# Kernel tuning notes

Measured on AMD Instinct MI355X. Metric: run time of the kernel, lower is better.

The kernel has to match this reference:

```python
import jax, jax.numpy as jnp
import numpy as np

N_NODES = 50000
N_EDGES = 800000
HEADS = 4
NEG_SLOPE = 0.2  # DGL GATConv default and act1 slope


def _gat_layer(x, src, dst, W, al, ar, b, n_nodes, heads, dh):
    # x: [N, Fin] -> proj: [N, H, Dh]
    proj = (x @ W).reshape(n_nodes, heads, dh)
    el = jnp.einsum('nhd,hd->nh', proj, al)  # [N, H]
    er = jnp.einsum('nhd,hd->nh', proj, ar)  # [N, H]
    e = jax.nn.leaky_relu(el[src] + er[dst], NEG_SLOPE)  # [E, H]
    # segment softmax over incoming edges of each dst node
    m = jax.ops.segment_max(e, dst, num_segments=n_nodes)
    m = jnp.where(jnp.isfinite(m), m, jnp.zeros_like(m))
    ex = jnp.exp(e - m[dst])
    s = jax.ops.segment_sum(ex, dst, num_segments=n_nodes)
    alpha = ex / (s[dst] + 1e-9)  # [E, H]
    msg = proj[src] * alpha[:, :, None]  # [E, H, Dh]
    out = jax.ops.segment_sum(msg, dst, num_segments=n_nodes)  # [N, H, Dh]
    return out.reshape(n_nodes, heads * dh) + b


def setup_inputs() -> dict:
    key = jax.random.key(0)
    ks = jax.random.split(key, 10)
    d = {
        'init_emb': jax.random.normal(ks[0], (N_NODES, 300), jnp.float32) * 0.1,
        'W1': jax.random.normal(ks[1], (300, 400), jnp.float32) * (1.0 / np.sqrt(300)),
        'al1': jax.random.normal(ks[2], (HEADS, 100), jnp.float32) * 0.1,
        'ar1': jax.random.normal(ks[3], (HEADS, 100), jnp.float32) * 0.1,
        'b1': jnp.zeros((400,), jnp.float32),
        'W2': jax.random.normal(ks[4], (400, 512), jnp.float32) * (1.0 / np.sqrt(400)),
        'al2': jax.random.normal(ks[5], (HEADS, 128), jnp.float32) * 0.1,
        'ar2': jax.random.normal(ks[6], (HEADS, 128), jnp.float32) * 0.1,
        'b2': jnp.zeros((512,), jnp.float32),
        'src': jax.random.randint(ks[7], (N_EDGES,), 0, N_NODES, jnp.int32),
        'dst': jax.random.randint(ks[8], (N_EDGES,), 0, N_NODES, jnp.int32),
    }
    return d


def reference(init_emb, W1, al1, ar1, b1, W2, al2, ar2, b2, src, dst):
    x = _gat_layer(init_emb, src, dst, W1, al1, ar1, b1, N_NODES, HEADS, 100)  # [N, 400]
    x = jax.nn.leaky_relu(x, NEG_SLOPE)  # act1
    x = _gat_layer(x, src, dst, W2, al2, ar2, b2, N_NODES, HEADS, 128)  # [N, 512]
    return x
```

## Files before the change

kernel.cpp:

```cpp
#include <hip/hip_runtime.h>
#include <math.h>
#include <stdint.h>

#define NN 50000
#define NE 800000
#define HEADS 4
#define MPAD 50048

typedef __attribute__((ext_vector_type(8))) short bf16x8;
typedef __attribute__((ext_vector_type(4))) float f32x4;

__device__ __forceinline__ uint32_t bf16rne(float x) {
  uint32_t b = __float_as_uint(x);
  return (b + 0x7FFFu + ((b >> 16) & 1u)) >> 16;
}
__device__ __forceinline__ float bflo(uint32_t v) {
  return __uint_as_float(v << 16);
}
__device__ __forceinline__ float bfhi(uint32_t v) {
  return __uint_as_float(v & 0xFFFF0000u);
}

__device__ __forceinline__ void pair_write(const float v[8], char* rowp, int q, int x) {
  uint32_t hi[8], lo[8];
#pragma unroll
  for (int j = 0; j < 8; ++j) {
    hi[j] = bf16rne(v[j]);
    float back = __uint_as_float(hi[j] << 16);
    lo[j] = bf16rne(v[j] - back);
  }
  uint4 hp, lp;
  hp.x = hi[0] | (hi[1] << 16);
  hp.y = hi[2] | (hi[3] << 16);
  hp.z = hi[4] | (hi[5] << 16);
  hp.w = hi[6] | (hi[7] << 16);
  lp.x = lo[0] | (lo[1] << 16);
  lp.y = lo[2] | (lo[3] << 16);
  lp.z = lo[4] | (lo[5] << 16);
  lp.w = lo[6] | (lo[7] << 16);
  *(uint4*)(rowp + ((q ^ x) << 4)) = hp;
  *(uint4*)(rowp + (((4 | q) ^ x) << 4)) = lp;
}

__global__ void hist_kernel(const int* __restrict__ dst, int* __restrict__ counts, int n) {
  int i = blockIdx.x * blockDim.x + threadIdx.x;
  if (i < n) atomicAdd(&counts[dst[i]], 1);
}

__global__ void scan_kernel(const int* __restrict__ counts, int* __restrict__ row_ptr,
                            int* __restrict__ cursor, int n) {
  __shared__ int wsum[16];
  const int lane = threadIdx.x & 63;
  const int w = threadIdx.x >> 6;
  int carry = 0;
  for (int start = 0; start < n; start += 1024) {
    int i = start + (int)threadIdx.x;
    int v = (i < n) ? counts[i] : 0;
    int x = v;
#pragma unroll
    for (int off = 1; off < 64; off <<= 1) {
      int t = __shfl_up(x, off);
      if (lane >= off) x += t;
    }
    if (lane == 63) wsum[w] = x;
    __syncthreads();
    if (w == 0 && lane < 16) {
      int s = wsum[lane];
#pragma unroll
      for (int off = 1; off < 16; off <<= 1) {
        int t = __shfl_up(s, off);
        if (lane >= off) s += t;
      }
      wsum[lane] = s;
    }
    __syncthreads();
    int woff = (w > 0) ? wsum[w - 1] : 0;
    int incl = x + woff;
    if (i < n) {
      int val = carry + incl - v;
      row_ptr[i] = val;
      cursor[i] = val;
    }
    carry += wsum[15];
    __syncthreads();
  }
  if (threadIdx.x == 0) row_ptr[n] = carry;
}

__global__ void scatter_kernel(const int* __restrict__ dst, const int* __restrict__ src,
                               int* __restrict__ cursor, int* __restrict__ srcs, int n) {
  int i = blockIdx.x * blockDim.x + threadIdx.x;
  if (i < n) {
    int pos = atomicAdd(&cursor[dst[i]], 1);
    srcs[pos] = src[i];
  }
}

__global__ void prepare_kernel(const float* __restrict__ X, unsigned short* __restrict__ A2,
                               const float* __restrict__ W1, unsigned short* __restrict__ B2a,
                               const float* __restrict__ W2, unsigned short* __restrict__ B2b) {
  const int bid = blockIdx.x;
  const int wv = threadIdx.x >> 6;
  const int t = threadIdx.x & 63;
  const int s = t >> 2, q = t & 3;
  const int kb = s * 32 + q * 8;
  if (bid < 1024) {
    if (t >= 40) return;
    const int nw = 1024 * 4;
    for (int m = bid * 4 + wv; m < MPAD; m += nw) {
      float v[8];
#pragma unroll
      for (int j = 0; j < 8; ++j) {
        int k = kb + j;
        v[j] = (m < NN && k < 300) ? X[(size_t)m * 300 + k] : 0.f;
      }
      pair_write(v, (char*)A2 + (size_t)m * 1280 + s * 128, q, m & 7);
    }
  } else if (bid < 1152) {
    if (t >= 40) return;
    const int n = (bid - 1024) * 4 + wv;
    float v[8];
#pragma unroll
    for (int j = 0; j < 8; ++j) {
      int k = kb + j;
      v[j] = (n < 400 && k < 300) ? W1[(size_t)k * 400 + n] : 0.f;
    }
    pair_write(v, (char*)B2a + (size_t)n * 1280 + s * 128, q, n & 7);
  } else {
    if (t >= 52) return;
    const int n = (bid - 1152) * 4 + wv;
    float v[8];
#pragma unroll
    for (int j = 0; j < 8; ++j) {
      int kp = kb + j;
      int h = kp / 104;
      int d = kp - h * 104;
      v[j] = (d < 100) ? W2[(size_t)(h * 100 + d) * 512 + n] : 0.f;
    }
    pair_write(v, (char*)B2b + (size_t)n * 1664 + s * 128, q, n & 7);
  }
}

__global__ __launch_bounds__(256, 2) void gemm_pairs(
    const unsigned short* __restrict__ A2, const unsigned short* __restrict__ B2,
    unsigned short* __restrict__ Ch, int M, int ksteps, int NstR, int RSc,
    int DHR, int DHP, int magic) {
  __shared__ unsigned short As[8192];
  __shared__ unsigned short Bs[8192];
  const int tid = threadIdx.x;
  const int w = tid >> 6, lane = tid & 63;
  const int wr = w >> 1, wc = w & 1;
  const int ln = lane & 15, quad = lane >> 4;
  const int m0 = blockIdx.y * 128, n0 = blockIdx.x * 128;
  const long strideB = (long)ksteps * 128;

  f32x4 acc[4][4];
#pragma unroll
  for (int mi = 0; mi < 4; ++mi)
#pragma unroll
    for (int ni = 0; ni < 4; ++ni) acc[mi][ni] = (f32x4){0.f, 0.f, 0.f, 0.f};

  const int xa = ln & 7;
  const int gA0 = (quad ^ xa) << 4, gA1 = ((4 | quad) ^ xa) << 4;

  for (int s = 0; s < ksteps; ++s) {
    const long sb = (long)s * 128;
#pragma unroll
    for (int j = 0; j < 4; ++j) {
      const int t16 = w * 4 + j;
      const int row = t16 * 8 + (lane >> 3);
      const int gran = lane & 7;
      const char* gpA = (const char*)A2 + (size_t)(m0 + row) * strideB + sb + gran * 16;
      const char* gpB = (const char*)B2 + (size_t)(n0 + row) * strideB + sb + gran * 16;
      __builtin_amdgcn_global_load_lds(
          (const __attribute__((address_space(1))) void*)gpA,
          (__attribute__((address_space(3))) void*)((char*)As + t16 * 1024), 16, 0, 0);
      __builtin_amdgcn_global_load_lds(
          (const __attribute__((address_space(1))) void*)gpB,
          (__attribute__((address_space(3))) void*)((char*)Bs + t16 * 1024), 16, 0, 0);
    }
    __syncthreads();
    bf16x8 ah[4], alo[4], bh[4], blo[4];
#pragma unroll
    for (int mi = 0; mi < 4; ++mi) {
      const int rA = wr * 64 + mi * 16 + ln;
      ah[mi] = *(const bf16x8*)((const char*)As + rA * 128 + gA0);
      alo[mi] = *(const bf16x8*)((const char*)As + rA * 128 + gA1);
    }
#pragma unroll
    for (int ni = 0; ni < 4; ++ni) {
      const int rB = wc * 64 + ni * 16 + ln;
      bh[ni] = *(const bf16x8*)((const char*)Bs + rB * 128 + gA0);
      blo[ni] = *(const bf16x8*)((const char*)Bs + rB * 128 + gA1);
    }
#pragma unroll
    for (int mi = 0; mi < 4; ++mi)
#pragma unroll
      for (int ni = 0; ni < 4; ++ni)
        acc[mi][ni] = __builtin_amdgcn_mfma_f32_16x16x32_bf16(ah[mi], bh[ni], acc[mi][ni], 0, 0, 0);
#pragma unroll
    for (int mi = 0; mi < 4; ++mi)
#pragma unroll
      for (int ni = 0; ni < 4; ++ni)
        acc[mi][ni] = __builtin_amdgcn_mfma_f32_16x16x32_bf16(ah[mi], blo[ni], acc[mi][ni], 0, 0, 0);
#pragma unroll
    for (int mi = 0; mi < 4; ++mi)
#pragma unroll
      for (int ni = 0; ni < 4; ++ni)
        acc[mi][ni] = __builtin_amdgcn_mfma_f32_16x16x32_bf16(alo[mi], bh[ni], acc[mi][ni], 0, 0, 0);
    __syncthreads();
  }
#pragma unroll
  for (int mi = 0; mi < 4; ++mi) {
#pragma unroll
    for (int r = 0; r < 4; ++r) {
      int gm = m0 + wr * 64 + mi * 16 + quad * 4 + r;
      if (gm < M) {
        unsigned short* crow = Ch + (size_t)gm * RSc;
#pragma unroll
        for (int ni = 0; ni < 4; ++ni) {
          int gn = n0 + wc * 64 + ni * 16 + ln;
          if (gn < NstR) {
            int h = (gn * magic) >> 12;
            int col = h * DHP + (gn - h * DHR);
            crow[col] = (unsigned short)bf16rne(acc[mi][ni][r]);
          }
        }
      }
    }
  }
}

template <int DHR, int DHP>
__global__ void el_er_kernel(const unsigned short* __restrict__ projh,
                             const float* __restrict__ al, const float* __restrict__ ar,
                             float* __restrict__ el, float* __restrict__ er) {
  int t = blockIdx.x * blockDim.x + threadIdx.x;
  if (t >= NN * HEADS) return;
  int h = t & (HEADS - 1);
  int n = t >> 2;
  const unsigned short* pr = projh + (size_t)n * (HEADS * DHP) + (size_t)h * DHP;
  const float* alh = al + h * DHR;
  const float* arh = ar + h * DHR;
  float sl = 0.f, sr = 0.f;
#pragma unroll 4
  for (int d = 0; d < DHR; d += 4) {
    uint2 pv = *(const uint2*)&pr[d];
    float p0 = bflo(pv.x), p1 = bfhi(pv.x), p2 = bflo(pv.y), p3 = bfhi(pv.y);
    float4 av = *(const float4*)&alh[d];
    float4 rv = *(const float4*)&arh[d];
    sl += p0 * av.x + p1 * av.y + p2 * av.z + p3 * av.w;
    sr += p0 * rv.x + p1 * rv.y + p2 * rv.z + p3 * rv.w;
  }
  el[t] = sl;
  er[t] = sr;
}

template <int DHP, int DHR, bool ACT, bool EMIT>
__global__ __launch_bounds__(256) void aggregate4(
    const unsigned short* __restrict__ projh, const float* __restrict__ el,
    const float* __restrict__ er, const float* __restrict__ bias,
    const int* __restrict__ row_ptr, const int* __restrict__ srcs,
    float* __restrict__ out, unsigned short* __restrict__ a2) {
  constexpr int LPH = DHP / 8;
  constexpr int RS = HEADS * DHP * 2;
  const int lane = threadIdx.x & 63;
  const int wid = blockIdx.x * 4 + (threadIdx.x >> 6);
  const int nw = gridDim.x * 4;
  const int e16 = lane >> 2, hp = lane & 3;
  int head;
  if constexpr (LPH == 16) head = lane >> 4;
  else head = (lane * 5) >> 6;
  const int u = lane - head * LPH;
  const bool active = lane < 4 * LPH;
  const int laneByte = active ? head * (DHP * 2) + u * 16 : 0;
  const char* pb = (const char*)projh;

  float bv[8];
  const int d0 = u * 8;
#pragma unroll
  for (int j = 0; j < 8; ++j)
    bv[j] = (active && d0 + j < DHR) ? bias[head * DHR + d0 + j] : 0.f;

  for (int node = wid; node < NN; node += nw) {
    const int beg = row_ptr[node], end = row_ptr[node + 1];
    const float er_p = er[node * 4 + hp];

    float acc[8];
#pragma unroll
    for (int j = 0; j < 8; ++j) acc[j] = 0.f;
    float lsum = 0.f;

    int i = beg;
    int rem = end - beg;
    int sE = 0;
    float elv = 0.f;
    if (rem > 0 && e16 < rem) {
      sE = srcs[i + e16];
      elv = el[sE * 4 + hp];
    }
    while (rem > 0) {
      const int take = rem < 16 ? rem : 16;
      float ev = elv + er_p;
      ev = fmaxf(ev, 0.2f * ev);
      const float pv_ = (e16 < take) ? __expf(ev) : 0.f;
      const int off_ = sE * RS;
      const int i2 = i + take;
      const int rem2 = rem - take;
      int sEn = 0;
      float elvn = 0.f;
      if (rem2 > 0 && e16 < rem2) {
        sEn = srcs[i2 + e16];
        elvn = el[sEn * 4 + hp];
      }
      if (take == 16) {
#pragma unroll
        for (int e = 0; e < 16; ++e) {
          const int sl = e * 4 + head;
          const float pv = __shfl(pv_, sl);
          const int off = __shfl(off_, sl);
          uint4 q = *(const uint4*)(pb + (uint32_t)(off + laneByte));
          lsum += pv;
          acc[0] += pv * bflo(q.x);
          acc[1] += pv * bfhi(q.x);
          acc[2] += pv * bflo(q.y);
          acc[3] += pv * bfhi(q.y);
          acc[4] += pv * bflo(q.z);
          acc[5] += pv * bfhi(q.z);
          acc[6] += pv * bflo(q.w);
          acc[7] += pv * bfhi(q.w);
        }
      } else {
        for (int e = 0; e < take; ++e) {
          const int sl = e * 4 + head;
          const float pv = __shfl(pv_, sl);
          const int off = __shfl(off_, sl);
          uint4 q = *(const uint4*)(pb + (uint32_t)(off + laneByte));
          lsum += pv;
          acc[0] += pv * bflo(q.x);
          acc[1] += pv * bfhi(q.x);
          acc[2] += pv * bflo(q.y);
          acc[3] += pv * bfhi(q.y);
          acc[4] += pv * bflo(q.z);
          acc[5] += pv * bfhi(q.z);
          acc[6] += pv * bflo(q.w);
          acc[7] += pv * bfhi(q.w);
        }
      }
      sE = sEn;
      elv = elvn;
      i = i2;
      rem = rem2;
    }

    const float inv = 1.f / (lsum + 1e-9f);
    if (active) {
      float o[8];
#pragma unroll
      for (int j = 0; j < 8; ++j) {
        float v = acc[j] * inv + bv[j];
        if (ACT) v = (v > 0.f) ? v : 0.2f * v;
        o[j] = (d0 + j < DHR) ? v : 0.f;
      }
      if constexpr (EMIT) {
        const int kp = head * DHP + u * 8;
        const int s2 = kp >> 5, q2 = (kp >> 3) & 3;
        pair_write(o, (char*)a2 + (size_t)node * 1664 + s2 * 128, q2, node & 7);
      } else {
        float* orow = out + (size_t)node * (HEADS * DHR) + head * DHR + d0;
        *(float4*)orow = make_float4(o[0], o[1], o[2], o[3]);
        if (d0 + 7 < DHR) *(float4*)(orow + 4) = make_float4(o[4], o[5], o[6], o[7]);
      }
    }
  }
}

extern "C" void kernel_launch(void* const* d_in, const int* in_sizes, int n_in,
                              void* d_out, int out_size, void* d_ws, size_t ws_size,
                              hipStream_t stream) {
  const float* init_emb = (const float*)d_in[0];
  const float* W1 = (const float*)d_in[1];
  const float* al1 = (const float*)d_in[2];
  const float* ar1 = (const float*)d_in[3];
  const float* b1 = (const float*)d_in[4];
  const float* W2 = (const float*)d_in[5];
  const float* al2 = (const float*)d_in[6];
  const float* ar2 = (const float*)d_in[7];
  const float* b2 = (const float*)d_in[8];
  const int* src = (const int*)d_in[9];
  const int* dst = (const int*)d_in[10];
  float* out = (float*)d_out;

  char* ws = (char*)d_ws;
  size_t off = 0;
  auto alloc = [&](size_t bytes) {
    void* p = ws + off;
    off += (bytes + 255) & ~((size_t)255);
    return p;
  };
  unsigned short* projh = (unsigned short*)alloc((size_t)NN * 512 * 2);
  float* el = (float*)alloc((size_t)NN * HEADS * 4);
  float* er = (float*)alloc((size_t)NN * HEADS * 4);
  unsigned short* B2a = (unsigned short*)alloc((size_t)512 * 10 * 128);
  unsigned short* B2b = (unsigned short*)alloc((size_t)512 * 13 * 128);
  int* row_ptr = (int*)alloc((size_t)(NN + 1) * 4);
  int* counts = (int*)alloc((size_t)NN * 4);
  int* cursor = (int*)alloc((size_t)NN * 4);
  int* srcs = (int*)alloc((size_t)NE * 4);
  unsigned short* A2 = (unsigned short*)d_out;

  prepare_kernel<<<1280, 256, 0, stream>>>(init_emb, A2, W1, B2a, W2, B2b);

  hipMemsetAsync(counts, 0, (size_t)NN * 4, stream);
  hist_kernel<<<(NE + 255) / 256, 256, 0, stream>>>(dst, counts, NE);
  scan_kernel<<<1, 1024, 0, stream>>>(counts, row_ptr, cursor, NN);
  scatter_kernel<<<(NE + 255) / 256, 256, 0, stream>>>(dst, src, cursor, srcs, NE);

  gemm_pairs<<<dim3(4, MPAD / 128), 256, 0, stream>>>(A2, B2a, projh, NN, 10, 400, 416, 100, 104, 41);
  el_er_kernel<100, 104><<<(NN * HEADS + 255) / 256, 256, 0, stream>>>(projh, al1, ar1, el, er);
  aggregate4<104, 100, true, true><<<2048, 256, 0, stream>>>(projh, el, er, b1, row_ptr,
                                                             srcs, nullptr, A2);

  gemm_pairs<<<dim3(4, MPAD / 128), 256, 0, stream>>>(A2, B2b, projh, NN, 13, 512, 512, 128, 128, 32);
  el_er_kernel<128, 128><<<(NN * HEADS + 255) / 256, 256, 0, stream>>>(projh, al2, ar2, el, er);
  aggregate4<128, 128, false, false><<<2048, 256, 0, stream>>>(projh, el, er, b2, row_ptr,
                                                               srcs, out, nullptr);
}
```

Baseline: 775.3 us.

## Fuse histogram into prepare kernel, use nontemporal stores, raise GEMM occupancy

Folds the dst histogram atomics into extra blocks of the prepare kernel, removing one kernel launch and letting the histogram overlap with the operand packing. Switches the aggregate kernels' final output writes to nontemporal stores so streamed results do not pollute the cache. Raises the GEMM launch bound from 2 to 3 blocks per CU, which may force register spilling in exchange for more occupancy.

```diff
diff --git a/kernel.cpp b/kernel.cpp
--- a/kernel.cpp
+++ b/kernel.cpp
@@ -9,6 +9,7 @@
 
 typedef __attribute__((ext_vector_type(8))) short bf16x8;
 typedef __attribute__((ext_vector_type(4))) float f32x4;
+typedef __attribute__((ext_vector_type(4))) unsigned int u32x4;
 
 __device__ __forceinline__ uint32_t bf16rne(float x) {
   uint32_t b = __float_as_uint(x);
@@ -21,7 +22,7 @@
   return __uint_as_float(v & 0xFFFF0000u);
 }
 
-__device__ __forceinline__ void pair_write(const float v[8], char* rowp, int q, int x) {
+__device__ __forceinline__ void pair_pack(const float v[8], u32x4& hp, u32x4& lp) {
   uint32_t hi[8], lo[8];
 #pragma unroll
   for (int j = 0; j < 8; ++j) {
@@ -29,7 +30,6 @@
     float back = __uint_as_float(hi[j] << 16);
     lo[j] = bf16rne(v[j] - back);
   }
-  uint4 hp, lp;
   hp.x = hi[0] | (hi[1] << 16);
   hp.y = hi[2] | (hi[3] << 16);
   hp.z = hi[4] | (hi[5] << 16);
@@ -38,13 +38,20 @@
   lp.y = lo[2] | (lo[3] << 16);
   lp.z = lo[4] | (lo[5] << 16);
   lp.w = lo[6] | (lo[7] << 16);
-  *(uint4*)(rowp + ((q ^ x) << 4)) = hp;
-  *(uint4*)(rowp + (((4 | q) ^ x) << 4)) = lp;
-}
-
-__global__ void hist_kernel(const int* __restrict__ dst, int* __restrict__ counts, int n) {
-  int i = blockIdx.x * blockDim.x + threadIdx.x;
-  if (i < n) atomicAdd(&counts[dst[i]], 1);
+}
+
+__device__ __forceinline__ void pair_write(const float v[8], char* rowp, int q, int x) {
+  u32x4 hp, lp;
+  pair_pack(v, hp, lp);
+  *(u32x4*)(rowp + ((q ^ x) << 4)) = hp;
+  *(u32x4*)(rowp + (((4 | q) ^ x) << 4)) = lp;
+}
+
+__device__ __forceinline__ void pair_write_nt(const float v[8], char* rowp, int q, int x) {
+  u32x4 hp, lp;
+  pair_pack(v, hp, lp);
+  __builtin_nontemporal_store(hp, (u32x4*)(rowp + ((q ^ x) << 4)));
+  __builtin_nontemporal_store(lp, (u32x4*)(rowp + (((4 | q) ^ x) << 4)));
 }
 
 __global__ void scan_kernel(const int* __restrict__ counts, int* __restrict__ row_ptr,
@@ -98,8 +105,14 @@
 
 __global__ void prepare_kernel(const float* __restrict__ X, unsigned short* __restrict__ A2,
                                const float* __restrict__ W1, unsigned short* __restrict__ B2a,
-                               const float* __restrict__ W2, unsigned short* __restrict__ B2b) {
+                               const float* __restrict__ W2, unsigned short* __restrict__ B2b,
+                               const int* __restrict__ dst, int* __restrict__ counts) {
   const int bid = blockIdx.x;
+  if (bid >= 1280) {
+    int e = (bid - 1280) * 256 + (int)threadIdx.x;
+    if (e < NE) atomicAdd(&counts[dst[e]], 1);
+    return;
+  }
   const int wv = threadIdx.x >> 6;
   const int t = threadIdx.x & 63;
   const int s = t >> 2, q = t & 3;
@@ -141,7 +154,7 @@
   }
 }
 
-__global__ __launch_bounds__(256, 2) void gemm_pairs(
+__global__ __launch_bounds__(256, 3) void gemm_pairs(
     const unsigned short* __restrict__ A2, const unsigned short* __restrict__ B2,
     unsigned short* __restrict__ Ch, int M, int ksteps, int NstR, int RSc,
     int DHR, int DHP, int magic) {
@@ -319,7 +332,7 @@
           const int sl = e * 4 + head;
           const float pv = __shfl(pv_, sl);
           const int off = __shfl(off_, sl);
-          uint4 q = *(const uint4*)(pb + (uint32_t)(off + laneByte));
+          u32x4 q = *(const u32x4*)(pb + (uint32_t)(off + laneByte));
           lsum += pv;
           acc[0] += pv * bflo(q.x);
           acc[1] += pv * bfhi(q.x);
@@ -335,7 +348,7 @@
           const int sl = e * 4 + head;
           const float pv = __shfl(pv_, sl);
           const int off = __shfl(off_, sl);
-          uint4 q = *(const uint4*)(pb + (uint32_t)(off + laneByte));
+          u32x4 q = *(const u32x4*)(pb + (uint32_t)(off + laneByte));
           lsum += pv;
           acc[0] += pv * bflo(q.x);
           acc[1] += pv * bfhi(q.x);
@@ -365,11 +378,15 @@
       if constexpr (EMIT) {
         const int kp = head * DHP + u * 8;
         const int s2 = kp >> 5, q2 = (kp >> 3) & 3;
-        pair_write(o, (char*)a2 + (size_t)node * 1664 + s2 * 128, q2, node & 7);
+        pair_write_nt(o, (char*)a2 + (size_t)node * 1664 + s2 * 128, q2, node & 7);
       } else {
         float* orow = out + (size_t)node * (HEADS * DHR) + head * DHR + d0;
-        *(float4*)orow = make_float4(o[0], o[1], o[2], o[3]);
-        if (d0 + 7 < DHR) *(float4*)(orow + 4) = make_float4(o[4], o[5], o[6], o[7]);
+        f32x4 o0 = {o[0], o[1], o[2], o[3]};
+        __builtin_nontemporal_store(o0, (f32x4*)orow);
+        if (d0 + 7 < DHR) {
+          f32x4 o1 = {o[4], o[5], o[6], o[7]};
+          __builtin_nontemporal_store(o1, (f32x4*)(orow + 4));
+        }
       }
     }
   }
@@ -409,10 +426,9 @@
   int* srcs = (int*)alloc((size_t)NE * 4);
   unsigned short* A2 = (unsigned short*)d_out;
 
-  prepare_kernel<<<1280, 256, 0, stream>>>(init_emb, A2, W1, B2a, W2, B2b);
-
   hipMemsetAsync(counts, 0, (size_t)NN * 4, stream);
-  hist_kernel<<<(NE + 255) / 256, 256, 0, stream>>>(dst, counts, NE);
+  prepare_kernel<<<1280 + (NE + 255) / 256, 256, 0, stream>>>(init_emb, A2, W1, B2a, W2, B2b,
+                                                              dst, counts);
   scan_kernel<<<1, 1024, 0, stream>>>(counts, row_ptr, cursor, NN);
   scatter_kernel<<<(NE + 255) / 256, 256, 0, stream>>>(dst, src, cursor, srcs, NE);
 
```

After: 745.1 us. -3.9%, faster.
